# Optimization experiments

Hardware: AMD Instinct MI355X
Metric: run time of the kernel (lower is better)

The kernel has to match this reference:

```python
import jax, jax.numpy as jnp
import numpy as np

N_WIRES = 25                    # odd -> RX on wire 0, then SingleExcitation on (1,2),(3,4),...,(23,24)
DIM = 2 ** N_WIRES              # 33_554_432 amplitudes
N_THETA = (N_WIRES + 1) // 2    # 13


def _apply_rx(state, th, wire):
    """Apply RX(th) = [[cos, -i sin], [-i sin, cos]] (half-angle) to `wire`.
    PennyLane convention: wire 0 is the most-significant bit of the amplitude index."""
    c = jnp.cos(th * 0.5)
    ms = -1j * jnp.sin(th * 0.5)
    st = state.reshape(2 ** wire, 2, -1)          # [pre, 2, post]
    s0, s1 = st[:, 0], st[:, 1]
    new = jnp.stack([c * s0 + ms * s1, ms * s0 + c * s1], axis=1)
    return new.reshape(-1)


def _apply_single_excitation(state, phi, wire):
    """SingleExcitation(phi) on wires [wire, wire+1]: rotates the |01>,|10> subspace
    by angle phi/2; |00>,|11> untouched."""
    c = jnp.cos(phi * 0.5)
    s = jnp.sin(phi * 0.5)
    st = state.reshape(2 ** wire, 2, 2, -1)       # [pre, q_i, q_{i+1}, post]
    a00, a01, a10, a11 = st[:, 0, 0], st[:, 0, 1], st[:, 1, 0], st[:, 1, 1]
    n01 = c * a01 - s * a10
    n10 = s * a01 + c * a10
    new = jnp.stack([jnp.stack([a00, n01], axis=1),
                     jnp.stack([n10, a11], axis=1)], axis=1)
    return new.reshape(-1)


def setup_inputs() -> dict:
    key = jax.random.key(0)
    kf, kt = jax.random.split(key)
    feature = jax.random.normal(kf, (DIM,), dtype=jnp.float32)
    # he_normal init on shape (13, 1): std = sqrt(2 / fan_in) with fan_in = 13
    theta = jax.random.normal(kt, (N_THETA, 1), dtype=jnp.float32) * np.sqrt(2.0 / N_THETA)
    return {"feature": feature, "theta": theta}


def reference(feature, theta) -> jnp.ndarray:
    # AmplitudeEmbedding with pad_with=0.0: pad (no-op here, len == 2^n) then L2-normalize
    state = (feature / jnp.linalg.norm(feature)).astype(jnp.complex64)
    # odd wire count: RX(theta[0][0]) on wire 0, start pair gates at wire 1
    state = _apply_rx(state, theta[0, 0], 0)
    for i in range(1, N_WIRES, 2):                # i = 1,3,...,23 -> theta[0..11]
        state = _apply_single_excitation(state, theta[i // 2, 0], i)
    return jnp.real(state)
```

## Files before the change

kernel.cpp:

```cpp
#include <hip/hip_runtime.h>
#include <math.h>


typedef float f32x4 __attribute__((ext_vector_type(4)));

static __device__ __forceinline__ float4 nt_load4(const float* p) {
    f32x4 v = __builtin_nontemporal_load((const f32x4*)p);
    return *(float4*)&v;
}
static __device__ __forceinline__ void nt_store4(float* p, float4 v) {
    __builtin_nontemporal_store(*(f32x4*)&v, (f32x4*)p);
}

static __device__ __forceinline__ void rot4(float4& a, float4& b, float c, float s) {
    float4 na, nb;
    na.x = c*a.x - s*b.x;  nb.x = s*a.x + c*b.x;
    na.y = c*a.y - s*b.y;  nb.y = s*a.y + c*b.y;
    na.z = c*a.z - s*b.z;  nb.z = s*a.z + c*b.z;
    na.w = c*a.w - s*b.w;  nb.w = s*a.w + c*b.w;
    a = na; b = nb;
}

static __device__ __forceinline__ float4 shflx4(float4 v, int m) {
    float4 r;
    r.x = __shfl_xor(v.x, m, 64);
    r.y = __shfl_xor(v.y, m, 64);
    r.z = __shfl_xor(v.z, m, 64);
    r.w = __shfl_xor(v.w, m, 64);
    return r;
}

template <int NR>
static __device__ __forceinline__ void rotshfl(float4* f, int sh, float c, float s, int lane) {
    const int pv = (lane >> sh) & 3;
    const bool act = (pv == 1) || (pv == 2);
    const float cl = act ? c : 1.0f;
    const float sl = act ? ((pv == 1) ? -s : s) : 0.0f;
    const int m = 3 << sh;
#pragma unroll
    for (int k = 0; k < NR; ++k) {
        float4 p = shflx4(f[k], m);
        float4 n;
        n.x = fmaf(sl, p.x, cl * f[k].x);
        n.y = fmaf(sl, p.y, cl * f[k].y);
        n.z = fmaf(sl, p.z, cl * f[k].z);
        n.w = fmaf(sl, p.w, cl * f[k].w);
        f[k] = n;
    }
}

__global__ __launch_bounds__(256, 2) void qnn_p1(const float* __restrict__ in,
                                                 const float* __restrict__ theta,
                                                 float* __restrict__ out,
                                                 double* __restrict__ partials) {
    __shared__ __align__(16) float4 lds[4096];
    __shared__ double red[4];
    const int t = threadIdx.x, lane = t & 63, w2 = t >> 6;
    const long gfb = (long)blockIdx.x << 12;

    float c0,s0,c1,s1,c2,s2,c3,s3,c4,s4,c5,s5,c6,s6;
    { float th;
      th=0.5f*theta[11]; c0=cosf(th); s0=sinf(th);
      th=0.5f*theta[10]; c1=cosf(th); s1=sinf(th);
      th=0.5f*theta[9];  c2=cosf(th); s2=sinf(th);
      th=0.5f*theta[8];  c3=cosf(th); s3=sinf(th);
      th=0.5f*theta[7];  c4=cosf(th); s4=sinf(th);
      th=0.5f*theta[6];  c5=cosf(th); s5=sinf(th);
      th=0.5f*theta[5];  c6=cosf(th); s6=sinf(th); }

    float4 f[16];
#pragma unroll
    for (int k = 0; k < 16; ++k) {
        const int s_ = (w2 << 10) | (k << 6) | lane;
        f[k] = nt_load4(in + ((gfb + s_) << 2));
    }
    double acc = 0.0;
#pragma unroll
    for (int k = 0; k < 16; ++k)
        acc += (double)f[k].x*f[k].x + (double)f[k].y*f[k].y
             + (double)f[k].z*f[k].z + (double)f[k].w*f[k].w;

#pragma unroll
    for (int k = 0; k < 16; ++k) {
        float ny = c0*f[k].y - s0*f[k].z;
        float nz = s0*f[k].y + c0*f[k].z;
        f[k].y = ny; f[k].z = nz;
    }
    rotshfl<16>(f, 0, c1, s1, lane);
    rotshfl<16>(f, 2, c2, s2, lane);
    rotshfl<16>(f, 4, c3, s3, lane);
#pragma unroll
    for (int hi = 0; hi < 16; hi += 4)
        rot4(f[hi + 1], f[hi + 2], c4, s4);
#pragma unroll
    for (int lo = 0; lo < 4; ++lo)
        rot4(f[4 + lo], f[8 + lo], c5, s5);

#pragma unroll
    for (int k = 0; k < 16; ++k)
        lds[(w2 << 10) | (k << 6) | lane] = f[k];
    __syncthreads();
#pragma unroll
    for (int m = 0; m < 16; ++m)
        f[m] = lds[(m << 8) | (w2 << 6) | lane];
#pragma unroll
    for (int lo = 0; lo < 4; ++lo)
        rot4(f[4 + lo], f[8 + lo], c6, s6);

#pragma unroll
    for (int m = 0; m < 16; ++m) {
        const int s_ = (m << 8) | (w2 << 6) | lane;
        *(float4*)(out + ((gfb + s_) << 2)) = f[m];
    }

#pragma unroll
    for (int off = 32; off > 0; off >>= 1) acc += __shfl_down(acc, off, 64);
    if (lane == 0) red[w2] = acc;
    __syncthreads();
    if (t == 0)
        partials[blockIdx.x] = red[0] + red[1] + red[2] + red[3];
}

__global__ void qnn_norm(const double* __restrict__ partials,
                         const float* __restrict__ theta,
                         double* __restrict__ scale) {
    __shared__ double w[4];
    const int t = threadIdx.x;
    double acc = 0.0;
    for (int i = t; i < 2048; i += 256) acc += partials[i];
#pragma unroll
    for (int off = 32; off > 0; off >>= 1) acc += __shfl_down(acc, off, 64);
    if ((t & 63) == 0) w[t >> 6] = acc;
    __syncthreads();
    if (t == 0) {
        double tot = w[0] + w[1] + w[2] + w[3];
        *scale = (double)cosf(0.5f * theta[0]) / sqrt(tot);
    }
}

__global__ __launch_bounds__(1024, 4) void qnn_high(float* __restrict__ buf,
                                                    const float* __restrict__ theta,
                                                    const double* __restrict__ scale) {
    __shared__ __align__(16) float4 lds[8192];
    const int t = threadIdx.x, lane = t & 63, w = t >> 6;
    const int bid = blockIdx.x;
    const int b24 = bid >> 9, mid = bid & 511;
    const long gq = ((long)b24 << 22) | ((long)mid << 3);

    float c7,s7,c8,s8,c9,s9,c10,s10,c11,s11;
    { float th;
      th=0.5f*theta[4]; c7 =cosf(th); s7 =sinf(th);
      th=0.5f*theta[3]; c8 =cosf(th); s8 =sinf(th);
      th=0.5f*theta[2]; c9 =cosf(th); s9 =sinf(th);
      th=0.5f*theta[1]; c10=cosf(th); s10=sinf(th);
      th=0.5f*theta[0]; c11=cosf(th); s11=sinf(th); }
    const float sc = (float)(*scale);

    float4 f[8];
#pragma unroll
    for (int k = 0; k < 8; ++k) {
        const int s_ = (k << 10) | t;
        f[k] = *(const float4*)(buf + ((gq | ((long)(s_ >> 3) << 12) | (s_ & 7)) << 2));
    }
    rotshfl<8>(f, 3, c7, s7, lane);
    rot4(f[2], f[4], c11, s11);
    rot4(f[3], f[5], c11, s11);
#pragma unroll
    for (int k = 0; k < 8; ++k) lds[(k << 10) | t] = f[k];
    __syncthreads();

    {
        const int base = ((lane >> 5) << 12) | (w << 8) | (lane & 31);
#pragma unroll
        for (int b = 0; b < 8; ++b) f[b] = lds[base | (b << 5)];
        rot4(f[1], f[2], c8, s8);
        rot4(f[5], f[6], c8, s8);
#pragma unroll
        for (int b = 0; b < 8; ++b) lds[base | (b << 5)] = f[b];
    }
    __syncthreads();

    {
        const int base = ((w >> 1) << 10) | ((w & 1) << 6) | lane;
#pragma unroll
        for (int b = 0; b < 8; ++b) f[b] = lds[base | (b << 7)];
        rot4(f[1], f[2], c9, s9);
        rot4(f[5], f[6], c9, s9);
#pragma unroll
        for (int b = 0; b < 8; ++b) lds[base | (b << 7)] = f[b];
    }
    __syncthreads();

    {
        const int base = ((w >> 3) << 12) | ((w & 7) << 6) | lane;
#pragma unroll
        for (int k = 0; k < 8; ++k) f[k] = lds[base | (k << 9)];
        rot4(f[1], f[2], c10, s10);
        rot4(f[5], f[6], c10, s10);
#pragma unroll
        for (int k = 0; k < 8; ++k) {
            const int s_ = base | (k << 9);
            float4 v = f[k];
            v.x *= sc; v.y *= sc; v.z *= sc; v.w *= sc;
            nt_store4(buf + ((gq | ((long)(s_ >> 3) << 12) | (s_ & 7)) << 2), v);
        }
    }
}

extern "C" void kernel_launch(void* const* d_in, const int* in_sizes, int n_in,
                              void* d_out, int out_size, void* d_ws, size_t ws_size,
                              hipStream_t stream) {
    const float* in = (const float*)d_in[0];
    const float* theta = (const float*)d_in[1];
    float* out = (float*)d_out;
    double* part = (double*)d_ws;
    double* scale = part + 2048;

    qnn_p1<<<2048, 256, 0, stream>>>(in, theta, out, part);
    qnn_norm<<<1, 256, 0, stream>>>(part, theta, scale);
    qnn_high<<<1024, 1024, 0, stream>>>(out, theta, scale);
}
```

Before: 104.5 us.

## Process two tiles per block with early loads and restructure high-wire pass

```diff
diff --git a/kernel.cpp b/kernel.cpp
--- a/kernel.cpp
+++ b/kernel.cpp
@@ -10,6 +10,10 @@
 }
 static __device__ __forceinline__ void nt_store4(float* p, float4 v) {
     __builtin_nontemporal_store(*(f32x4*)&v, (f32x4*)p);
+}
+
+static __device__ __forceinline__ void bar_lgkm() {
+    asm volatile("s_waitcnt lgkmcnt(0)\n\ts_barrier" ::: "memory");
 }
 
 static __device__ __forceinline__ void rot4(float4& a, float4& b, float c, float s) {
@@ -56,7 +60,8 @@
     __shared__ __align__(16) float4 lds[4096];
     __shared__ double red[4];
     const int t = threadIdx.x, lane = t & 63, w2 = t >> 6;
-    const long gfb = (long)blockIdx.x << 12;
+    const long gA = (long)blockIdx.x << 13;
+    const long gB = gA + 4096;
 
     float c0,s0,c1,s1,c2,s2,c3,s3,c4,s4,c5,s5,c6,s6;
     { float th;
@@ -68,12 +73,14 @@
       th=0.5f*theta[6];  c5=cosf(th); s5=sinf(th);
       th=0.5f*theta[5];  c6=cosf(th); s6=sinf(th); }
 
-    float4 f[16];
-#pragma unroll
-    for (int k = 0; k < 16; ++k) {
-        const int s_ = (w2 << 10) | (k << 6) | lane;
-        f[k] = nt_load4(in + ((gfb + s_) << 2));
-    }
+    float4 f[16], g[16];
+#pragma unroll
+    for (int k = 0; k < 16; ++k)
+        f[k] = nt_load4(in + ((gA + ((w2 << 10) | (k << 6) | lane)) << 2));
+#pragma unroll
+    for (int k = 0; k < 16; ++k)
+        g[k] = nt_load4(in + ((gB + ((w2 << 10) | (k << 6) | lane)) << 2));
+
     double acc = 0.0;
 #pragma unroll
     for (int k = 0; k < 16; ++k)
@@ -90,33 +97,55 @@
     rotshfl<16>(f, 2, c2, s2, lane);
     rotshfl<16>(f, 4, c3, s3, lane);
 #pragma unroll
-    for (int hi = 0; hi < 16; hi += 4)
-        rot4(f[hi + 1], f[hi + 2], c4, s4);
-#pragma unroll
-    for (int lo = 0; lo < 4; ++lo)
-        rot4(f[4 + lo], f[8 + lo], c5, s5);
-
-#pragma unroll
-    for (int k = 0; k < 16; ++k)
-        lds[(w2 << 10) | (k << 6) | lane] = f[k];
-    __syncthreads();
+    for (int hi = 0; hi < 16; hi += 4) rot4(f[hi+1], f[hi+2], c4, s4);
+#pragma unroll
+    for (int lo = 0; lo < 4; ++lo)     rot4(f[4+lo], f[8+lo], c5, s5);
+
+#pragma unroll
+    for (int k = 0; k < 16; ++k) lds[(w2 << 10) | (k << 6) | lane] = f[k];
+    bar_lgkm();
+#pragma unroll
+    for (int m = 0; m < 16; ++m) f[m] = lds[(m << 8) | (w2 << 6) | lane];
+#pragma unroll
+    for (int lo = 0; lo < 4; ++lo) rot4(f[4+lo], f[8+lo], c6, s6);
 #pragma unroll
     for (int m = 0; m < 16; ++m)
-        f[m] = lds[(m << 8) | (w2 << 6) | lane];
-#pragma unroll
-    for (int lo = 0; lo < 4; ++lo)
-        rot4(f[4 + lo], f[8 + lo], c6, s6);
-
-#pragma unroll
-    for (int m = 0; m < 16; ++m) {
-        const int s_ = (m << 8) | (w2 << 6) | lane;
-        *(float4*)(out + ((gfb + s_) << 2)) = f[m];
-    }
+        *(float4*)(out + ((gA + ((m << 8) | (w2 << 6) | lane)) << 2)) = f[m];
+
+#pragma unroll
+    for (int k = 0; k < 16; ++k)
+        acc += (double)g[k].x*g[k].x + (double)g[k].y*g[k].y
+             + (double)g[k].z*g[k].z + (double)g[k].w*g[k].w;
+#pragma unroll
+    for (int k = 0; k < 16; ++k) {
+        float ny = c0*g[k].y - s0*g[k].z;
+        float nz = s0*g[k].y + c0*g[k].z;
+        g[k].y = ny; g[k].z = nz;
+    }
+    rotshfl<16>(g, 0, c1, s1, lane);
+    rotshfl<16>(g, 2, c2, s2, lane);
+    rotshfl<16>(g, 4, c3, s3, lane);
+#pragma unroll
+    for (int hi = 0; hi < 16; hi += 4) rot4(g[hi+1], g[hi+2], c4, s4);
+#pragma unroll
+    for (int lo = 0; lo < 4; ++lo)     rot4(g[4+lo], g[8+lo], c5, s5);
+
+    bar_lgkm();
+#pragma unroll
+    for (int k = 0; k < 16; ++k) lds[(w2 << 10) | (k << 6) | lane] = g[k];
+    bar_lgkm();
+#pragma unroll
+    for (int m = 0; m < 16; ++m) g[m] = lds[(m << 8) | (w2 << 6) | lane];
+#pragma unroll
+    for (int lo = 0; lo < 4; ++lo) rot4(g[4+lo], g[8+lo], c6, s6);
+#pragma unroll
+    for (int m = 0; m < 16; ++m)
+        *(float4*)(out + ((gB + ((m << 8) | (w2 << 6) | lane)) << 2)) = g[m];
 
 #pragma unroll
     for (int off = 32; off > 0; off >>= 1) acc += __shfl_down(acc, off, 64);
     if (lane == 0) red[w2] = acc;
-    __syncthreads();
+    bar_lgkm();
     if (t == 0)
         partials[blockIdx.x] = red[0] + red[1] + red[2] + red[3];
 }
@@ -127,7 +156,7 @@
     __shared__ double w[4];
     const int t = threadIdx.x;
     double acc = 0.0;
-    for (int i = t; i < 2048; i += 256) acc += partials[i];
+    for (int i = t; i < 1024; i += 256) acc += partials[i];
 #pragma unroll
     for (int off = 32; off > 0; off >>= 1) acc += __shfl_down(acc, off, 64);
     if ((t & 63) == 0) w[t >> 6] = acc;
@@ -138,14 +167,14 @@
     }
 }
 
-__global__ __launch_bounds__(1024, 4) void qnn_high(float* __restrict__ buf,
-                                                    const float* __restrict__ theta,
-                                                    const double* __restrict__ scale) {
+__global__ __launch_bounds__(512, 2) void qnn_high(float* __restrict__ buf,
+                                                   const float* __restrict__ theta,
+                                                   const double* __restrict__ scale) {
     __shared__ __align__(16) float4 lds[8192];
-    const int t = threadIdx.x, lane = t & 63, w = t >> 6;
-    const int bid = blockIdx.x;
-    const int b24 = bid >> 9, mid = bid & 511;
-    const long gq = ((long)b24 << 22) | ((long)mid << 3);
+    const int t = threadIdx.x, lane = t & 63, w3 = t >> 6;
+    const int mid = blockIdx.x;
+    const long gqA = (long)mid << 3;
+    const long gqB = (1L << 22) | ((long)mid << 3);
 
     float c7,s7,c8,s8,c9,s9,c10,s10,c11,s11;
     { float th;
@@ -156,54 +185,63 @@
       th=0.5f*theta[0]; c11=cosf(th); s11=sinf(th); }
     const float sc = (float)(*scale);
 
-    float4 f[8];
-#pragma unroll
-    for (int k = 0; k < 8; ++k) {
-        const int s_ = (k << 10) | t;
-        f[k] = *(const float4*)(buf + ((gq | ((long)(s_ >> 3) << 12) | (s_ & 7)) << 2));
-    }
-    rotshfl<8>(f, 3, c7, s7, lane);
-    rot4(f[2], f[4], c11, s11);
-    rot4(f[3], f[5], c11, s11);
-#pragma unroll
-    for (int k = 0; k < 8; ++k) lds[(k << 10) | t] = f[k];
-    __syncthreads();
-
-    {
-        const int base = ((lane >> 5) << 12) | (w << 8) | (lane & 31);
-#pragma unroll
-        for (int b = 0; b < 8; ++b) f[b] = lds[base | (b << 5)];
-        rot4(f[1], f[2], c8, s8);
-        rot4(f[5], f[6], c8, s8);
-#pragma unroll
-        for (int b = 0; b < 8; ++b) lds[base | (b << 5)] = f[b];
-    }
-    __syncthreads();
-
-    {
-        const int base = ((w >> 1) << 10) | ((w & 1) << 6) | lane;
-#pragma unroll
-        for (int b = 0; b < 8; ++b) f[b] = lds[base | (b << 7)];
-        rot4(f[1], f[2], c9, s9);
-        rot4(f[5], f[6], c9, s9);
-#pragma unroll
-        for (int b = 0; b < 8; ++b) lds[base | (b << 7)] = f[b];
-    }
-    __syncthreads();
-
-    {
-        const int base = ((w >> 3) << 12) | ((w & 7) << 6) | lane;
-#pragma unroll
-        for (int k = 0; k < 8; ++k) f[k] = lds[base | (k << 9)];
-        rot4(f[1], f[2], c10, s10);
-        rot4(f[5], f[6], c10, s10);
-#pragma unroll
-        for (int k = 0; k < 8; ++k) {
-            const int s_ = base | (k << 9);
-            float4 v = f[k];
-            v.x *= sc; v.y *= sc; v.z *= sc; v.w *= sc;
-            nt_store4(buf + ((gq | ((long)(s_ >> 3) << 12) | (s_ & 7)) << 2), v);
-        }
+    const int rbase = (w3 << 10) | ((lane >> 5) << 9) | (lane & 31);
+
+    float4 f[16], g[16];
+#pragma unroll
+    for (int k = 0; k < 16; ++k) {
+        const int s_ = (k << 9) | t;
+        f[k] = *(const float4*)(buf + ((gqA | ((long)(s_ >> 3) << 12) | (s_ & 7)) << 2));
+    }
+#pragma unroll
+    for (int k = 0; k < 16; ++k) {
+        const int s_ = (k << 9) | t;
+        g[k] = *(const float4*)(buf + ((gqB | ((long)(s_ >> 3) << 12) | (s_ & 7)) << 2));
+    }
+
+    rotshfl<16>(f, 3, c7, s7, lane);
+#pragma unroll
+    for (int hi = 0; hi < 16; hi += 4) rot4(f[hi+1], f[hi+2], c10, s10);
+#pragma unroll
+    for (int lo = 0; lo < 4; ++lo)     rot4(f[4+lo], f[8+lo], c11, s11);
+#pragma unroll
+    for (int k = 0; k < 16; ++k) lds[(k << 9) | t] = f[k];
+    bar_lgkm();
+#pragma unroll
+    for (int m = 0; m < 16; ++m) f[m] = lds[rbase | (m << 5)];
+#pragma unroll
+    for (int hi = 0; hi < 16; hi += 4) rot4(f[hi+1], f[hi+2], c8, s8);
+#pragma unroll
+    for (int lo = 0; lo < 4; ++lo)     rot4(f[4+lo], f[8+lo], c9, s9);
+#pragma unroll
+    for (int m = 0; m < 16; ++m) {
+        const int s_ = rbase | (m << 5);
+        float4 v = f[m];
+        v.x *= sc; v.y *= sc; v.z *= sc; v.w *= sc;
+        nt_store4(buf + ((gqA | ((long)(s_ >> 3) << 12) | (s_ & 7)) << 2), v);
+    }
+
+    rotshfl<16>(g, 3, c7, s7, lane);
+#pragma unroll
+    for (int hi = 0; hi < 16; hi += 4) rot4(g[hi+1], g[hi+2], c10, s10);
+#pragma unroll
+    for (int lo = 0; lo < 4; ++lo)     rot4(g[4+lo], g[8+lo], c11, s11);
+    bar_lgkm();
+#pragma unroll
+    for (int k = 0; k < 16; ++k) lds[(k << 9) | t] = g[k];
+    bar_lgkm();
+#pragma unroll
+    for (int m = 0; m < 16; ++m) g[m] = lds[rbase | (m << 5)];
+#pragma unroll
+    for (int hi = 0; hi < 16; hi += 4) rot4(g[hi+1], g[hi+2], c8, s8);
+#pragma unroll
+    for (int lo = 0; lo < 4; ++lo)     rot4(g[4+lo], g[8+lo], c9, s9);
+#pragma unroll
+    for (int m = 0; m < 16; ++m) {
+        const int s_ = rbase | (m << 5);
+        float4 v = g[m];
+        v.x *= sc; v.y *= sc; v.z *= sc; v.w *= sc;
+        nt_store4(buf + ((gqB | ((long)(s_ >> 3) << 12) | (s_ & 7)) << 2), v);
     }
 }
 
@@ -214,9 +252,9 @@
     const float* theta = (const float*)d_in[1];
     float* out = (float*)d_out;
     double* part = (double*)d_ws;
-    double* scale = part + 2048;
-
-    qnn_p1<<<2048, 256, 0, stream>>>(in, theta, out, part);
+    double* scale = part + 1024;
+
+    qnn_p1<<<1024, 256, 0, stream>>>(in, theta, out, part);
     qnn_norm<<<1, 256, 0, stream>>>(part, theta, scale);
-    qnn_high<<<1024, 1024, 0, stream>>>(out, theta, scale);
-}
+    qnn_high<<<512, 512, 0, stream>>>(out, theta, scale);
+}
```

Result: faster. 97.96 us (-6.2%).
